# Optimization experiments

Hardware: AMD Instinct MI355X
Metric: run time of the kernel (lower is better)

The kernel has to match this reference:

```python
import jax, jax.numpy as jnp
import numpy as np

B, S, D_IN, D_OUT = 1, 2048, 4096, 4096
N_HEADS, N_KV = 32, 8
HEAD_DIM = D_OUT // N_HEADS  # 128
GROUP = N_HEADS // N_KV      # 4


def _rope_tables(seq_len, head_dim, base=10000.0):
    inv = 1.0 / (base ** (np.arange(0, head_dim, 2, dtype=np.float32) / head_dim))
    t = np.arange(seq_len, dtype=np.float32)
    ang = np.outer(t, inv)                       # [S, hd/2]
    ang = np.concatenate([ang, ang], axis=-1)    # [S, hd]
    return jnp.asarray(np.cos(ang)), jnp.asarray(np.sin(ang))


def setup_inputs() -> dict:
    key = jax.random.key(0)
    kx, kq, kk, kv, ko = jax.random.split(key, 5)
    cos, sin = _rope_tables(S, HEAD_DIM)
    sc = 0.02
    return {
        "x": jax.random.normal(kx, (B, S, D_IN), dtype=jnp.float32),
        "cos": cos,
        "sin": sin,
        "Wq": jax.random.normal(kq, (D_OUT, D_IN), dtype=jnp.float32) * sc,
        "Wk": jax.random.normal(kk, (N_KV * HEAD_DIM, D_IN), dtype=jnp.float32) * sc,
        "Wv": jax.random.normal(kv, (N_KV * HEAD_DIM, D_IN), dtype=jnp.float32) * sc,
        "Wo": jax.random.normal(ko, (D_OUT, D_OUT), dtype=jnp.float32) * sc,
    }


def _apply_rope(t, cos, sin):
    # t: [b, h, s, hd]; cos/sin: [s, hd] -> rotate-half RoPE
    hd = t.shape[-1]
    x1, x2 = t[..., : hd // 2], t[..., hd // 2 :]
    rotated = jnp.concatenate([-x2, x1], axis=-1)
    return t * cos[None, None] + rotated * sin[None, None]


def reference(x, cos, sin, Wq, Wk, Wv, Wo):
    b, s, _ = x.shape
    q = (x @ Wq.T).reshape(b, s, N_HEADS, HEAD_DIM).transpose(0, 2, 1, 3)  # [b,H,s,hd]
    k = (x @ Wk.T).reshape(b, s, N_KV, HEAD_DIM).transpose(0, 2, 1, 3)     # [b,G,s,hd]
    v = (x @ Wv.T).reshape(b, s, N_KV, HEAD_DIM).transpose(0, 2, 1, 3)
    q = _apply_rope(q, cos, sin)
    k = _apply_rope(k, cos, sin)
    k = jnp.repeat(k, GROUP, axis=1)  # [b,H,s,hd]
    v = jnp.repeat(v, GROUP, axis=1)
    scores = jnp.einsum("bhqd,bhkd->bhqk", q, k)
    causal = jnp.triu(jnp.ones((s, s), dtype=bool), k=1)
    scores = jnp.where(causal[None, None], -jnp.inf, scores)
    attn = jax.nn.softmax(scores / jnp.sqrt(jnp.float32(HEAD_DIM)), axis=-1)
    ctx = jnp.einsum("bhqk,bhkd->bhqd", attn, v)
    ctx = ctx.transpose(0, 2, 1, 3).reshape(b, s, D_OUT)
    return ctx @ Wo.T
```

## Files before the change

kernel.cpp:

```cpp
#include <hip/hip_runtime.h>


typedef __bf16 bf16;
typedef __bf16 bf16x4 __attribute__((ext_vector_type(4)));
typedef __bf16 bf16x8 __attribute__((ext_vector_type(8)));
typedef float  f32x4  __attribute__((ext_vector_type(4)));

#define S_LEN   2048
#define DMODEL  4096
#define QKV_N   6144
#define K_OFF   4096
#define V_OFF   5120
#define HD      128
#define ATT_SCALE 0.08838834764831845f

__device__ __forceinline__ void gload16(const bf16* g, bf16* l) {
    __builtin_amdgcn_global_load_lds(
        (__attribute__((address_space(1))) void*)(g),
        (__attribute__((address_space(3))) void*)(l),
        16, 0, 0);
}

__global__ __launch_bounds__(256) void cast_f32_bf16(const float* __restrict__ in,
                                                     bf16* __restrict__ out, int n4) {
    int i = blockIdx.x * 256 + threadIdx.x;
    if (i >= n4) return;
    float4 v = reinterpret_cast<const float4*>(in)[i];
    bf16x4 o;
    o[0] = (bf16)v.x; o[1] = (bf16)v.y; o[2] = (bf16)v.z; o[3] = (bf16)v.w;
    reinterpret_cast<bf16x4*>(out)[i] = o;
}

template <typename OutT>
__global__ __launch_bounds__(256) void gemm_bt(const bf16* __restrict__ A,
                                               const bf16* __restrict__ B,
                                               OutT* __restrict__ C,
                                               int M, int N, int K, int ldc) {
    __shared__ bf16 As[128 * 32];
    __shared__ bf16 Bs[128 * 32];
    const int t    = threadIdx.x;
    const int wave = t >> 6, lane = t & 63;
    const int quad = lane >> 4, l15 = lane & 15;
    const int wm = (wave >> 1) * 64, wn = (wave & 1) * 64;
    const int bm = blockIdx.y * 128, bn = blockIdx.x * 128;

    f32x4 acc[4][4];
#pragma unroll
    for (int i = 0; i < 4; ++i)
#pragma unroll
        for (int j = 0; j < 4; ++j) acc[i][j] = (f32x4){0.f, 0.f, 0.f, 0.f};

    const int soff  = t * 8;
    const int arow0 = soff >> 5;
    const int acol  = soff & 31;

    for (int k0 = 0; k0 < K; k0 += 32) {
        __syncthreads();
#pragma unroll
        for (int it = 0; it < 2; ++it) {
            gload16(A + (size_t)(bm + arow0 + it * 64) * K + k0 + acol,
                    As + it * 2048 + wave * 512);
            gload16(B + (size_t)(bn + arow0 + it * 64) * K + k0 + acol,
                    Bs + it * 2048 + wave * 512);
        }
        __syncthreads();

        bf16x8 af[4], bfb[4];
#pragma unroll
        for (int i = 0; i < 4; ++i)
            af[i] = *reinterpret_cast<const bf16x8*>(&As[(wm + i * 16 + l15) * 32 + quad * 8]);
#pragma unroll
        for (int j = 0; j < 4; ++j)
            bfb[j] = *reinterpret_cast<const bf16x8*>(&Bs[(wn + j * 16 + l15) * 32 + quad * 8]);
#pragma unroll
        for (int i = 0; i < 4; ++i)
#pragma unroll
            for (int j = 0; j < 4; ++j)
                acc[i][j] = __builtin_amdgcn_mfma_f32_16x16x32_bf16(af[i], bfb[j], acc[i][j], 0, 0, 0);
    }

#pragma unroll
    for (int i = 0; i < 4; ++i) {
        const int m0 = bm + wm + i * 16 + quad * 4;
#pragma unroll
        for (int j = 0; j < 4; ++j) {
            const int n = bn + wn + j * 16 + l15;
#pragma unroll
            for (int r = 0; r < 4; ++r)
                C[(size_t)(m0 + r) * ldc + n] = (OutT)acc[i][j][r];
        }
    }
}

__global__ __launch_bounds__(256) void rope_kernel(bf16* __restrict__ qkv,
                                                   const float* __restrict__ cosT,
                                                   const float* __restrict__ sinT) {
    const int col = blockIdx.x * 256 + threadIdx.x;
    if (col >= 40 * 64) return;
    const int row  = blockIdx.y;
    const int head = col >> 6, d = col & 63;
    const size_t base = (size_t)row * QKV_N + head * 128 + d;
    const float x1 = (float)qkv[base];
    const float x2 = (float)qkv[base + 64];
    const float c  = cosT[row * 128 + d];
    const float s  = sinT[row * 128 + d];
    qkv[base]      = (bf16)(x1 * c - x2 * s);
    qkv[base + 64] = (bf16)(x2 * c + x1 * s);
}

__global__ __launch_bounds__(256) void transpose_v(const bf16* __restrict__ qkv,
                                                   bf16* __restrict__ vt) {
    __shared__ bf16 T[64][72];
    const int c0 = blockIdx.x * 64;
    const int s0 = blockIdx.y * 64;
    const int t  = threadIdx.x;
#pragma unroll
    for (int it = 0; it < 2; ++it) {
        const int sl = (t >> 3) + it * 32;
        const int c8 = (t & 7) * 8;
        bf16x8 v = *reinterpret_cast<const bf16x8*>(
            qkv + (size_t)(s0 + sl) * QKV_N + V_OFF + c0 + c8);
        *reinterpret_cast<bf16x8*>(&T[sl][c8]) = v;
    }
    __syncthreads();
#pragma unroll
    for (int it = 0; it < 2; ++it) {
        const int cl = (t >> 3) + it * 32;
        const int s8 = (t & 7) * 8;
        bf16x8 o;
#pragma unroll
        for (int e = 0; e < 8; ++e) o[e] = T[s8 + e][cl];
        *reinterpret_cast<bf16x8*>(vt + (size_t)(c0 + cl) * S_LEN + s0 + s8) = o;
    }
}

__global__ __launch_bounds__(512) void flash_attn(const bf16* __restrict__ qkv,
                                                  const bf16* __restrict__ vt,
                                                  bf16* __restrict__ ctx) {
    const int blk   = blockIdx.x;
    const int qtile = 15 - (blk >> 5);
    const int h     = blk & 31;
    const int kh    = h >> 2;
    const int q0    = qtile * 128;
    const int t     = threadIdx.x;
    const int wave  = t >> 6, lane = t & 63;
    const int quad  = lane >> 4, l15 = lane & 15;

    __shared__ bf16 Ks[64 * 128];
    __shared__ bf16 Vs[128 * 64];
    __shared__ bf16 Ps[8 * 16 * 72];

    const bf16* Qb  = qkv + h * HD;
    const bf16* Kb  = qkv + K_OFF + kh * HD;
    const bf16* Vth = vt + (size_t)kh * HD * S_LEN;

    const int qrow_a = q0 + wave * 16 + l15;
    bf16x8 qf[4];
#pragma unroll
    for (int kk = 0; kk < 4; ++kk)
        qf[kk] = *reinterpret_cast<const bf16x8*>(
            Qb + (size_t)qrow_a * QKV_N + kk * 32 + quad * 8);

    float m_i[4], l_i[4];
    f32x4 o_acc[8];
#pragma unroll
    for (int r = 0; r < 4; ++r) { m_i[r] = -1e30f; l_i[r] = 0.f; }
#pragma unroll
    for (int dt = 0; dt < 8; ++dt) o_acc[dt] = (f32x4){0.f, 0.f, 0.f, 0.f};

    const int myrow = q0 + wave * 16 + quad * 4;
    bf16* PsW = Ps + wave * (16 * 72);

    for (int kv0 = 0; kv0 < q0 + 128; kv0 += 64) {
        __syncthreads();
#pragma unroll
        for (int it = 0; it < 2; ++it) {
            const int rb = wave * 8 + it * 4;
            const int r  = rb + (lane >> 4);
            const int cg = (lane & 15) ^ (r & 15);
            gload16(Kb + (size_t)(kv0 + r) * QKV_N + cg * 8, Ks + rb * 128);
        }
#pragma unroll
        for (int it = 0; it < 2; ++it) {
            const int db = wave * 16 + it * 8;
            const int d  = db + (lane >> 3);
            const int cg = (lane & 7) ^ (d & 7);
            gload16(Vth + (size_t)d * S_LEN + kv0 + cg * 8, Vs + db * 64);
        }
        __syncthreads();

        float sv[4][4];
        const bool need_mask = (kv0 + 63) > q0;
#pragma unroll
        for (int j = 0; j < 4; ++j) {
            f32x4 s = (f32x4){0.f, 0.f, 0.f, 0.f};
#pragma unroll
            for (int kk = 0; kk < 4; ++kk) {
                const int cd = kk * 4 + quad;
                bf16x8 kf = *reinterpret_cast<const bf16x8*>(
                    &Ks[(j * 16 + l15) * 128 + ((cd ^ l15) & 15) * 8]);
                s = __builtin_amdgcn_mfma_f32_16x16x32_bf16(qf[kk], kf, s, 0, 0, 0);
            }
            if (need_mask) {
#pragma unroll
                for (int r = 0; r < 4; ++r)
                    sv[j][r] = ((kv0 + j * 16 + l15) <= (myrow + r))
                                   ? s[r] * ATT_SCALE : -1e30f;
            } else {
#pragma unroll
                for (int r = 0; r < 4; ++r) sv[j][r] = s[r] * ATT_SCALE;
            }
        }

        float al[4];
#pragma unroll
        for (int r = 0; r < 4; ++r) {
            float mt = fmaxf(fmaxf(sv[0][r], sv[1][r]), fmaxf(sv[2][r], sv[3][r]));
#pragma unroll
            for (int off = 1; off < 16; off <<= 1) mt = fmaxf(mt, __shfl_xor(mt, off));
            const float mn = fmaxf(m_i[r], mt);
            al[r] = __expf(m_i[r] - mn);
            m_i[r] = mn;
            float rs = 0.f;
#pragma unroll
            for (int j = 0; j < 4; ++j) {
                const float p = __expf(sv[j][r] - mn);
                rs += p;
                PsW[(quad * 4 + r) * 72 + j * 16 + l15] = (bf16)p;
            }
#pragma unroll
            for (int off = 1; off < 16; off <<= 1) rs += __shfl_xor(rs, off);
            l_i[r] = l_i[r] * al[r] + rs;
        }

#pragma unroll
        for (int dt = 0; dt < 8; ++dt) {
            o_acc[dt][0] *= al[0]; o_acc[dt][1] *= al[1];
            o_acc[dt][2] *= al[2]; o_acc[dt][3] *= al[3];
        }

        bf16x8 pa[2];
        pa[0] = *reinterpret_cast<const bf16x8*>(&PsW[l15 * 72 + quad * 8]);
        pa[1] = *reinterpret_cast<const bf16x8*>(&PsW[l15 * 72 + 32 + quad * 8]);
#pragma unroll
        for (int dt = 0; dt < 8; ++dt) {
#pragma unroll
            for (int c = 0; c < 2; ++c) {
                const int ck = c * 4 + quad;
                bf16x8 vb = *reinterpret_cast<const bf16x8*>(
                    &Vs[(dt * 16 + l15) * 64 + ((ck ^ (l15 & 7)) & 7) * 8]);
                o_acc[dt] = __builtin_amdgcn_mfma_f32_16x16x32_bf16(pa[c], vb, o_acc[dt], 0, 0, 0);
            }
        }
    }

#pragma unroll
    for (int dt = 0; dt < 8; ++dt)
#pragma unroll
        for (int r = 0; r < 4; ++r)
            ctx[(size_t)(myrow + r) * DMODEL + h * HD + dt * 16 + l15] =
                (bf16)(o_acc[dt][r] / l_i[r]);
}

extern "C" void kernel_launch(void* const* d_in, const int* in_sizes, int n_in,
                              void* d_out, int out_size, void* d_ws, size_t ws_size,
                              hipStream_t stream) {
    const float* x    = (const float*)d_in[0];
    const float* cosT = (const float*)d_in[1];
    const float* sinT = (const float*)d_in[2];
    const float* Wq   = (const float*)d_in[3];
    const float* Wk   = (const float*)d_in[4];
    const float* Wv   = (const float*)d_in[5];
    const float* Wo   = (const float*)d_in[6];
    float* out = (float*)d_out;

    bf16* xb   = (bf16*)d_ws;
    bf16* Wqkv = xb   + (size_t)S_LEN * DMODEL;
    bf16* Wob  = Wqkv + (size_t)QKV_N * DMODEL;
    bf16* QKV  = Wob  + (size_t)DMODEL * DMODEL;
    bf16* ctx  = QKV  + (size_t)S_LEN * QKV_N;
    bf16* Vt   = ctx  + (size_t)S_LEN * DMODEL;

    cast_f32_bf16<<<(S_LEN * DMODEL / 4 + 255) / 256, 256, 0, stream>>>(x, xb, S_LEN * DMODEL / 4);
    cast_f32_bf16<<<(DMODEL * DMODEL / 4 + 255) / 256, 256, 0, stream>>>(Wq, Wqkv, DMODEL * DMODEL / 4);
    cast_f32_bf16<<<(1024 * DMODEL / 4 + 255) / 256, 256, 0, stream>>>(
        Wk, Wqkv + (size_t)4096 * DMODEL, 1024 * DMODEL / 4);
    cast_f32_bf16<<<(1024 * DMODEL / 4 + 255) / 256, 256, 0, stream>>>(
        Wv, Wqkv + (size_t)5120 * DMODEL, 1024 * DMODEL / 4);
    cast_f32_bf16<<<(DMODEL * DMODEL / 4 + 255) / 256, 256, 0, stream>>>(Wo, Wob, DMODEL * DMODEL / 4);

    gemm_bt<bf16><<<dim3(QKV_N / 128, S_LEN / 128), 256, 0, stream>>>(
        xb, Wqkv, QKV, S_LEN, QKV_N, DMODEL, QKV_N);

    rope_kernel<<<dim3(10, S_LEN), 256, 0, stream>>>(QKV, cosT, sinT);

    transpose_v<<<dim3(16, 32), 256, 0, stream>>>(QKV, Vt);

    flash_attn<<<dim3(16 * 32), 512, 0, stream>>>(QKV, Vt, ctx);

    gemm_bt<float><<<dim3(DMODEL / 128, S_LEN / 128), 256, 0, stream>>>(
        ctx, Wob, out, S_LEN, DMODEL, DMODEL, DMODEL);
}
```

Before: 557.6 us.

## Replace GEMM with 256x256 double-buffered, swizzled, XCD-remapped kernel

Swaps the simple 128x128 single-buffered GEMM for a 256x256-tile, 512-thread kernel with a 64-wide K step. Global-to-LDS loads go into two LDS buffers and are interleaved with MFMA compute, using explicit vmcnt waits and barriers. LDS layout uses an XOR swizzle to avoid bank conflicts, and block IDs are remapped across the 8 XCDs for better L2 locality. This targets the GEMM's exposed load latency and low data reuse, in exchange for much higher LDS use (128KB) and register pressure, plus fragile hand-written synchronisation.

```diff
diff --git a/kernel.cpp b/kernel.cpp
--- a/kernel.cpp
+++ b/kernel.cpp
@@ -32,62 +32,138 @@
 }
 
 template <typename OutT>
-__global__ __launch_bounds__(256) void gemm_bt(const bf16* __restrict__ A,
-                                               const bf16* __restrict__ B,
-                                               OutT* __restrict__ C,
-                                               int M, int N, int K, int ldc) {
-    __shared__ bf16 As[128 * 32];
-    __shared__ bf16 Bs[128 * 32];
+__global__ __launch_bounds__(512, 2) void gemm256(const bf16* __restrict__ A,
+                                                  const bf16* __restrict__ B,
+                                                  OutT* __restrict__ C,
+                                                  int M, int N, int K, int ldc) {
+    __shared__ bf16 Lsh[2 * 2 * 256 * 64];
     const int t    = threadIdx.x;
-    const int wave = t >> 6, lane = t & 63;
+    const int lane = t & 63;
+    const int wave = t >> 6;
     const int quad = lane >> 4, l15 = lane & 15;
-    const int wm = (wave >> 1) * 64, wn = (wave & 1) * 64;
-    const int bm = blockIdx.y * 128, bn = blockIdx.x * 128;
-
-    f32x4 acc[4][4];
-#pragma unroll
-    for (int i = 0; i < 4; ++i)
+    const int wm = wave >> 2, wn = wave & 3;
+
+    int bid = blockIdx.y * gridDim.x + blockIdx.x;
+    const int nwg = gridDim.x * gridDim.y;
+    {
+        const int q = nwg >> 3, r = nwg & 7;
+        const int x = bid & 7, i = bid >> 3;
+        bid = (x < r ? x * (q + 1) : r * (q + 1) + (x - r) * q) + i;
+    }
+    const int ntn = N >> 8;
+    const int bm  = (bid / ntn) << 8;
+    const int bn  = (bid % ntn) << 8;
+
+    const bf16* Ablk = A + (size_t)bm * K;
+    const bf16* Bblk = B + (size_t)bn * K;
+    const int NT = K >> 6;
+
+    bf16* L0A = Lsh;
+    bf16* L0B = Lsh + 16384;
+    bf16* L1A = Lsh + 32768;
+    bf16* L1B = Lsh + 49152;
+
+    {
+        #define STAGE_HALF(G, LR)                                              \
+            {                                                                  \
+                _Pragma("unroll")                                              \
+                for (int j = 0; j < 2; ++j) {                                  \
+                    const int r = j * 64 + (t >> 3);                           \
+                    const int c = ((t & 7) ^ ((t >> 3) & 7)) << 3;             \
+                    gload16((G) + (size_t)r * K + c,                           \
+                            (LR) + j * 4096 + ((t >> 6) << 9));                \
+                }                                                              \
+            }
+        STAGE_HALF(Ablk,                    L0A);
+        STAGE_HALF(Ablk + (size_t)128 * K,  L0A + 8192);
+        STAGE_HALF(Bblk,                    L0B);
+        STAGE_HALF(Bblk + (size_t)128 * K,  L0B + 8192);
+        if (NT > 1) {
+            STAGE_HALF(Bblk + 64,                   L1B);
+            STAGE_HALF(Bblk + (size_t)128 * K + 64, L1B + 8192);
+        }
+        asm volatile("s_waitcnt vmcnt(0)");
+        __builtin_amdgcn_s_barrier();
+    }
+
+    f32x4 acc[8][4];
+#pragma unroll
+    for (int i = 0; i < 8; ++i)
 #pragma unroll
         for (int j = 0; j < 4; ++j) acc[i][j] = (f32x4){0.f, 0.f, 0.f, 0.f};
 
-    const int soff  = t * 8;
-    const int arow0 = soff >> 5;
-    const int acol  = soff & 31;
-
-    for (int k0 = 0; k0 < K; k0 += 32) {
-        __syncthreads();
-#pragma unroll
-        for (int it = 0; it < 2; ++it) {
-            gload16(A + (size_t)(bm + arow0 + it * 64) * K + k0 + acol,
-                    As + it * 2048 + wave * 512);
-            gload16(B + (size_t)(bn + arow0 + it * 64) * K + k0 + acol,
-                    Bs + it * 2048 + wave * 512);
-        }
-        __syncthreads();
-
-        bf16x8 af[4], bfb[4];
-#pragma unroll
-        for (int i = 0; i < 4; ++i)
-            af[i] = *reinterpret_cast<const bf16x8*>(&As[(wm + i * 16 + l15) * 32 + quad * 8]);
-#pragma unroll
-        for (int j = 0; j < 4; ++j)
-            bfb[j] = *reinterpret_cast<const bf16x8*>(&Bs[(wn + j * 16 + l15) * 32 + quad * 8]);
-#pragma unroll
-        for (int i = 0; i < 4; ++i)
-#pragma unroll
-            for (int j = 0; j < 4; ++j)
-                acc[i][j] = __builtin_amdgcn_mfma_f32_16x16x32_bf16(af[i], bfb[j], acc[i][j], 0, 0, 0);
-    }
-
-#pragma unroll
-    for (int i = 0; i < 4; ++i) {
-        const int m0 = bm + wm + i * 16 + quad * 4;
-#pragma unroll
-        for (int j = 0; j < 4; ++j) {
-            const int n = bn + wn + j * 16 + l15;
+    for (int tile = 0; tile < NT; ++tile) {
+        bf16* As = (tile & 1) ? L1A : L0A;
+        bf16* Bs = (tile & 1) ? L1B : L0B;
+        bf16* An = (tile & 1) ? L0A : L1A;
+        bf16x8 bfr[4][2];
+#pragma unroll
+        for (int q = 0; q < 4; ++q) {
+            bf16x8 af[2][2];
+#pragma unroll
+            for (int dm = 0; dm < 2; ++dm)
+#pragma unroll
+                for (int kk = 0; kk < 2; ++kk) {
+                    const int row = wm * 128 + q * 32 + dm * 16 + l15;
+                    const int ch  = (kk * 4 + quad) ^ (row & 7);
+                    af[dm][kk] = *reinterpret_cast<const bf16x8*>(
+                        &As[row * 64 + (ch << 3)]);
+                }
+            if (q == 0) {
+#pragma unroll
+                for (int n = 0; n < 4; ++n)
+#pragma unroll
+                    for (int kk = 0; kk < 2; ++kk) {
+                        const int row = wn * 64 + n * 16 + l15;
+                        const int ch  = (kk * 4 + quad) ^ (row & 7);
+                        bfr[n][kk] = *reinterpret_cast<const bf16x8*>(
+                            &Bs[row * 64 + (ch << 3)]);
+                    }
+                if (tile + 1 < NT)
+                    STAGE_HALF(Ablk + (size_t)(tile + 1) * 64, An);
+            } else if (q == 1) {
+                if (tile + 1 < NT)
+                    STAGE_HALF(Ablk + (size_t)128 * K + (size_t)(tile + 1) * 64,
+                               An + 8192);
+                if (tile + 2 < NT)
+                    STAGE_HALF(Bblk + (size_t)(tile + 2) * 64, Bs);
+            } else if (q == 2) {
+                if (tile + 2 < NT)
+                    STAGE_HALF(Bblk + (size_t)128 * K + (size_t)(tile + 2) * 64,
+                               Bs + 8192);
+            }
+            __builtin_amdgcn_s_barrier();
+            asm volatile("s_waitcnt lgkmcnt(0)");
+            __builtin_amdgcn_s_setprio(1);
+#pragma unroll
+            for (int dm = 0; dm < 2; ++dm)
+#pragma unroll
+                for (int n = 0; n < 4; ++n)
+#pragma unroll
+                    for (int kk = 0; kk < 2; ++kk)
+                        acc[q * 2 + dm][n] = __builtin_amdgcn_mfma_f32_16x16x32_bf16(
+                            af[dm][kk], bfr[n][kk], acc[q * 2 + dm][n], 0, 0, 0);
+            __builtin_amdgcn_s_setprio(0);
+            if (q < 3) {
+                __builtin_amdgcn_s_barrier();
+            } else {
+                if (tile < NT - 2) { asm volatile("s_waitcnt vmcnt(4)"); }
+                else               { asm volatile("s_waitcnt vmcnt(0)"); }
+                __builtin_amdgcn_s_barrier();
+            }
+        }
+    }
+    #undef STAGE_HALF
+
+#pragma unroll
+    for (int mf = 0; mf < 8; ++mf) {
+        const int row0 = bm + wm * 128 + mf * 16 + quad * 4;
+#pragma unroll
+        for (int nf = 0; nf < 4; ++nf) {
+            const int col = bn + wn * 64 + nf * 16 + l15;
 #pragma unroll
             for (int r = 0; r < 4; ++r)
-                C[(size_t)(m0 + r) * ldc + n] = (OutT)acc[i][j][r];
+                C[(size_t)(row0 + r) * ldc + col] = (OutT)acc[mf][nf][r];
         }
     }
 }
@@ -289,7 +365,7 @@
         Wv, Wqkv + (size_t)5120 * DMODEL, 1024 * DMODEL / 4);
     cast_f32_bf16<<<(DMODEL * DMODEL / 4 + 255) / 256, 256, 0, stream>>>(Wo, Wob, DMODEL * DMODEL / 4);
 
-    gemm_bt<bf16><<<dim3(QKV_N / 128, S_LEN / 128), 256, 0, stream>>>(
+    gemm256<bf16><<<dim3(QKV_N / 256, S_LEN / 256), 512, 0, stream>>>(
         xb, Wqkv, QKV, S_LEN, QKV_N, DMODEL, QKV_N);
 
     rope_kernel<<<dim3(10, S_LEN), 256, 0, stream>>>(QKV, cosT, sinT);
@@ -298,6 +374,6 @@
 
     flash_attn<<<dim3(16 * 32), 512, 0, stream>>>(QKV, Vt, ctx);
 
-    gemm_bt<float><<<dim3(DMODEL / 128, S_LEN / 128), 256, 0, stream>>>(
+    gemm256<float><<<dim3(DMODEL / 256, S_LEN / 256), 512, 0, stream>>>(
         ctx, Wob, out, S_LEN, DMODEL, DMODEL, DMODEL);
 }
```

Result: no change. 557.0 us (-0.1%).
